# Performance work log

Measured on AMD Instinct MI355X. Metric: run time of the kernel, lower is better.

The kernel has to match this reference:

```python
import jax, jax.numpy as jnp
import numpy as np

N_TOKEN = 267735
D_EMBED = 1024
D_PROJ = 1024
DIV_VAL = 4
CUTOFFS = [20000, 40000, 200000, N_TOKEN]   # cutoffs + [n_token]
ENDS = [0] + CUTOFFS                         # cutoff_ends
N_CLUSTERS = len(CUTOFFS) - 1                # 3
HEAD_SIZE = CUTOFFS[0] + N_CLUSTERS          # 20003
N = 1024                                     # len*bsz


def setup_inputs() -> dict:
    key = jax.random.key(0)
    ks = jax.random.split(key, 16)
    d_embs = [D_EMBED // DIV_VAL ** i for i in range(4)]  # 1024,256,64,16
    sizes = [HEAD_SIZE] + [ENDS[i + 1] - ENDS[i] for i in range(1, 4)]  # 20003,20000,160000,67735
    s = 0.02
    inp = {
        'hidden': jax.random.normal(ks[0], (N, D_PROJ), dtype=jnp.float32),
        'target': jax.random.randint(ks[1], (N,), 0, N_TOKEN, dtype=jnp.int32),
    }
    for i in range(4):
        inp[f'w{i}'] = jax.random.normal(ks[2 + 3 * i], (sizes[i], d_embs[i]), dtype=jnp.float32) * s
        inp[f'b{i}'] = jnp.zeros((sizes[i],), dtype=jnp.float32)
        inp[f'p{i}'] = jax.random.normal(ks[3 + 3 * i], (D_PROJ, d_embs[i]), dtype=jnp.float32) * s
    return inp


def _logit(h, w, b, p):
    # F.linear(hidden, proj.t()) -> h @ p ; F.linear(., weight, bias) -> @ w.T + b
    return (h @ p) @ w.T + b


def reference(hidden, target, w0, b0, p0, w1, b1, p1, w2, b2, p2, w3, b3, p3):
    head_lp = jax.nn.log_softmax(_logit(hidden, w0, b0, p0), axis=1)  # [N, HEAD_SIZE]
    tails = [(w1, b1, p1), (w2, b2, p2), (w3, b3, p3)]
    lps = []
    # shortlist cluster: gather target logprob directly from head
    t0 = jnp.clip(target, 0, CUTOFFS[0] - 1)
    lps.append(jnp.take_along_axis(head_lp, t0[:, None], axis=1)[:, 0])
    # tail clusters: small projected matmul + log_softmax + gather, combined with cluster logprob head_lp[:, -i]
    for i in range(1, 4):
        l, r = ENDS[i], ENDS[i + 1]
        ti = jnp.clip(target - l, 0, r - l - 1)
        tail_lp = jax.nn.log_softmax(_logit(hidden, *tails[i - 1]), axis=1)  # [N, r-l]
        lps.append(head_lp[:, -i] + jnp.take_along_axis(tail_lp, ti[:, None], axis=1)[:, 0])
    masks = [(target >= ENDS[i]) & (target < ENDS[i + 1]) for i in range(4)]
    logprob = jnp.select(masks, lps)
    return -logprob  # [N] per-token NLL, original order (keep_order=True)
```

## Files before the change

### kernel.cpp

```cpp
#include <hip/hip_runtime.h>
#include <hip/hip_bf16.h>
#include <math.h>

#define NTOK 1024
#define DPROJ 1024
#define PSTRIDE 1376
#define HEADS 20003
#define LOG2E 1.4426950408889634f
#define LN2   0.6931471805599453f
#define WSCALE (4.0f * LOG2E)
#define PSCALE 0.25f

#if __has_builtin(__builtin_amdgcn_exp2f)
#define EXP2(x) __builtin_amdgcn_exp2f(x)
#else
#define EXP2(x) exp2f(x)
#endif

#define MFMA8(a, b, c) __builtin_amdgcn_mfma_f32_16x16x32_fp8_fp8(a, b, c, 0, 0, 0)

typedef __attribute__((ext_vector_type(8))) short bf16x8;
typedef __attribute__((ext_vector_type(4))) float f32x4;
typedef long long i64;
typedef __attribute__((ext_vector_type(2))) long long i64x2;

__device__ __forceinline__ short f2bf(float f) {
    unsigned u = __float_as_uint(f);
    u += 0x7fffu + ((u >> 16) & 1u);
    return (short)(u >> 16);
}
__device__ __forceinline__ unsigned pk4fp8(float a, float b, float c, float d) {
    unsigned v = __builtin_amdgcn_cvt_pk_fp8_f32(a, b, 0, false);
    v = __builtin_amdgcn_cvt_pk_fp8_f32(c, d, v, true);
    return v;
}
__device__ __forceinline__ unsigned char fp8_1(float a) {
    return (unsigned char)(__builtin_amdgcn_cvt_pk_fp8_f32(a, a, 0, false) & 0xff);
}
__device__ __forceinline__ i64 wfrag(const float* wp) {
    float4 x = *(const float4*)(wp);
    float4 y = *(const float4*)(wp + 4);
    unsigned lo = pk4fp8(x.x * WSCALE, x.y * WSCALE, x.z * WSCALE, x.w * WSCALE);
    unsigned hi = pk4fp8(y.x * WSCALE, y.y * WSCALE, y.z * WSCALE, y.w * WSCALE);
    return (i64)(((unsigned long long)hi << 32) | lo);
}

#define NB0H 313
#define NB1T 157
#define NB2T 313
#define NB3T 133
#define NSLAB (NB0H + NB1T + NB2T + NB3T)

#define EB0N 20096
#define EB1N 20096
#define EB2N 160256
#define EB3N 68096
#define EBTOT (EB0N + EB1N + EB2N + EB3N)

__global__ __launch_bounds__(256) void prep(const float* __restrict__ hidden,
                                            const float* __restrict__ p0,
                                            const float* __restrict__ p1,
                                            const float* __restrict__ p2,
                                            const float* __restrict__ p3,
                                            const float* __restrict__ b0,
                                            const float* __restrict__ b1,
                                            const float* __restrict__ b2,
                                            const float* __restrict__ b3,
                                            short* __restrict__ hbP,
                                            short* __restrict__ pTbP0,
                                            short* __restrict__ pTbP1,
                                            short* __restrict__ pTbP2,
                                            short* __restrict__ pTbP3,
                                            float* __restrict__ sums,
                                            unsigned char* __restrict__ pk3,
                                            float* __restrict__ eb0,
                                            float* __restrict__ eb1,
                                            float* __restrict__ eb2,
                                            float* __restrict__ eb3) {
    __shared__ float tile[64][65];
    int bid = blockIdx.x, tid = threadIdx.x;
    if (bid >= 418) {
        int g = (bid - 418) * 256 + tid;
        if (g < EB0N) {
            eb0[g] = (g < HEADS) ? exp2f(b0[g] * LOG2E) : 0.f;
        } else if (g < EB0N + EB1N) {
            int i = g - EB0N;
            eb1[i] = (i < 20000) ? exp2f(b1[i] * LOG2E) : 0.f;
        } else if (g < EB0N + EB1N + EB2N) {
            int i = g - EB0N - EB1N;
            eb2[i] = (i < 160000) ? exp2f(b2[i] * LOG2E) : 0.f;
        } else if (g < EBTOT) {
            int i = g - EB0N - EB1N - EB2N;
            eb3[i] = (i < 67735) ? exp2f(b3[i] * LOG2E) : 0.f;
        }
        return;
    }
    if (bid == 416) {
        float4 z = {0.f, 0.f, 0.f, 0.f};
        #pragma unroll
        for (int i = 0; i < 4; ++i) *((float4*)sums + i * 256 + tid) = z;
        return;
    }
    if (bid == 417) {
        int4 z = {0, 0, 0, 0};
        #pragma unroll
        for (int i = 0; i < 8; ++i) *((int4*)pk3 + i * 256 + tid) = z;
        return;
    }
    if (bid < 64) {
        int tt = bid;
        #pragma unroll
        for (int q = 0; q < 8; ++q) {
            int fi = q * 256 + tid;
            int l = fi & 63;
            int row = tt * 16 + (l & 15);
            int kb = (fi >> 6) * 32 + (l >> 4) * 8;
            const float* hp = hidden + row * 1024 + kb;
            float4 x = *(const float4*)hp;
            float4 y = *(const float4*)(hp + 4);
            bf16x8 o;
            o[0]=f2bf(x.x); o[1]=f2bf(x.y); o[2]=f2bf(x.z); o[3]=f2bf(x.w);
            o[4]=f2bf(y.x); o[5]=f2bf(y.y); o[6]=f2bf(y.z); o[7]=f2bf(y.w);
            *(bf16x8*)(hbP + (size_t)tt * 16384 + fi * 8) = o;
        }
        return;
    }
    int lb = bid - 64;
    const float* p; short* dst; int d, kt, jb;
    if (lb < 256)      { p = p0; dst = pTbP0; d = 1024; kt = lb >> 4; jb = lb & 15; }
    else if (lb < 320) { lb -= 256; p = p1; dst = pTbP1; d = 256; kt = lb >> 2; jb = lb & 3; }
    else if (lb < 336) { lb -= 320; p = p2; dst = pTbP2; d = 64;  kt = lb; jb = 0; }
    else               { lb -= 336; p = p3; dst = pTbP3; d = 16;  kt = lb; jb = 0; }
    int k0 = kt * 64, j0 = jb * 64;
    int tx = tid & 63, ty = tid >> 6;
    #pragma unroll
    for (int rr = 0; rr < 16; ++rr) {
        int k = k0 + ty * 16 + rr;
        int j = j0 + tx;
        if (j < d) tile[ty * 16 + rr][tx] = p[k * d + j];
    }
    __syncthreads();
    int ch = tid >> 5;
    int jtl = ch >> 1, ksl = ch & 1;
    int jt = jb * 4 + jtl;
    if (jt * 16 < d) {
        #pragma unroll
        for (int li = 0; li < 2; ++li) {
            int l = (tid & 31) + li * 32;
            int jl = jtl * 16 + (l & 15);
            int kl = ksl * 32 + (l >> 4) * 8;
            bf16x8 o;
            #pragma unroll
            for (int e = 0; e < 8; ++e) o[e] = f2bf(tile[kl + e][jl]);
            *(bf16x8*)(dst + ((size_t)jt * 32 + kt * 2 + ksl) * 512 + l * 8) = o;
        }
    }
}

__global__ __launch_bounds__(256) void proj(const short* __restrict__ hbP,
                                            const short* __restrict__ pTbP0,
                                            const short* __restrict__ pTbP1,
                                            const short* __restrict__ pTbP2,
                                            const short* __restrict__ pTbP3,
                                            float* __restrict__ projf,
                                            unsigned char* __restrict__ pk0,
                                            unsigned char* __restrict__ pk1,
                                            unsigned char* __restrict__ pk2,
                                            unsigned char* __restrict__ pk3) {
    __shared__ float spackf[16][72];
    __shared__ unsigned char sp8[1024];
    int tt = blockIdx.x, jbG = blockIdx.y, tid = threadIdx.x;
    const short* pB; unsigned char* pkc; int d, KSp, coloff, jb;
    if (jbG < 16)      { pB = pTbP0; pkc = pk0; d = 1024; KSp = 32; coloff = 0;    jb = jbG; }
    else if (jbG < 20) { pB = pTbP1; pkc = pk1; d = 256;  KSp = 8;  coloff = 1024; jb = jbG - 16; }
    else if (jbG == 20){ pB = pTbP2; pkc = pk2; d = 64;   KSp = 2;  coloff = 1280; jb = 0; }
    else               { pB = pTbP3; pkc = pk3; d = 16;   KSp = 1;  coloff = 1344; jb = 0; }
    int w = tid >> 6, lane = tid & 63;
    int l16 = lane & 15, quad = lane >> 4;
    int jt = jb * 4 + w;
    if (jt * 16 < d) {
        const short* ap = hbP + ((size_t)tt * 32) * 512 + lane * 8;
        const short* bp = pB  + ((size_t)jt * 32) * 512 + lane * 8;
        f32x4 x0 = {0,0,0,0}, x1 = {0,0,0,0};
        #pragma unroll
        for (int ks = 0; ks < 16; ++ks) {
            bf16x8 a0 = *(const bf16x8*)(ap + ks * 512);
            bf16x8 b0 = *(const bf16x8*)(bp + ks * 512);
            bf16x8 a1 = *(const bf16x8*)(ap + (ks + 16) * 512);
            bf16x8 b1 = *(const bf16x8*)(bp + (ks + 16) * 512);
            x0 = __builtin_amdgcn_mfma_f32_16x16x32_bf16(a0, b0, x0, 0, 0, 0);
            x1 = __builtin_amdgcn_mfma_f32_16x16x32_bf16(a1, b1, x1, 0, 0, 0);
        }
        f32x4 acc = x0 + x1;
        int kk = w * 16 + l16;
        #pragma unroll
        for (int r = 0; r < 4; ++r) {
            int tok = quad * 4 + r;
            spackf[tok][kk] = acc[r];
            int idx;
            if (d > 16) idx = ((kk & 31) >> 3) * 256 + tok * 16 + (kk >> 5) * 8 + (kk & 7);
            else        idx = ((kk & 31) >> 3) * 128 + tok * 8 + (kk & 7);
            sp8[idx] = fp8_1(acc[r] * PSCALE);
        }
    }
    __syncthreads();
    int j0g = jb * 64;
    int dcols = min(64, d - j0g);
    {
        int row = tid >> 4, cb = (tid & 15) * 4;
        if (cb < dcols) {
            float4 v = *(const float4*)&spackf[row][cb];
            *(float4*)&projf[(tt * 16 + row) * PSTRIDE + coloff + j0g + cb] = v;
        }
    }
    {
        int nbytes = 16 * dcols;
        if (tid * 4 < nbytes) {
            unsigned char* gdst = pkc + ((size_t)tt * KSp + (j0g >> 5)) * 512;
            *(unsigned*)(gdst + tid * 4) = *(const unsigned*)(sp8 + tid * 4);
        }
    }
}

__device__ __forceinline__ void stage16k(const unsigned char* g, unsigned char* l,
                                         int wave, int lane) {
    const unsigned char* gs = g + wave * 4096 + lane * 16;
    unsigned char* ls = l + wave * 4096;
    #pragma unroll
    for (int i = 0; i < 4; ++i)
        __builtin_amdgcn_global_load_lds(
            (const __attribute__((address_space(1))) unsigned*)(gs + i * 1024),
            (__attribute__((address_space(3))) unsigned*)(ls + i * 1024), 16, 0, 0);
}

__device__ __forceinline__ void lse_head(const float* __restrict__ w,
                                         const float* __restrict__ eb,
                                         const unsigned char* __restrict__ pk,
                                         float* __restrict__ part, int bid,
                                         unsigned char (*sbuf)[16384], float* bsum) {
    int tid = threadIdx.x;
    int wave = tid >> 6, lane = tid & 63;
    int quad = lane >> 4, l16 = lane & 15;
    int v0 = bid * 64 + wave * 16;

    for (int i = tid; i < NTOK; i += 256) bsum[i] = 0.f;

    i64 areg[32];
    float ee[4];
    int va = v0 + l16;
    #pragma unroll
    for (int ks = 0; ks < 32; ++ks)
        areg[ks] = (va < HEADS) ? wfrag(w + (long)va * 1024 + ks * 32 + quad * 8) : 0;
    #pragma unroll
    for (int r = 0; r < 4; ++r)
        ee[r] = eb[v0 + quad * 4 + r];

    unsigned char* pA = sbuf[0];
    unsigned char* pB = sbuf[1];
    unsigned char* pS = sbuf[2];
    stage16k(pk, pA, wave, lane);
    stage16k(pk + 16384, pB, wave, lane);
    __syncthreads();
    for (int tt = 0; tt < 64; ++tt) {
        if (tt + 2 < 64) stage16k(pk + (size_t)(tt + 2) * 16384, pS, wave, lane);
        const unsigned char* sb = pA;
        f32x4 x0 = {0,0,0,0}, x1 = x0;
        __builtin_amdgcn_s_setprio(1);
        #pragma unroll
        for (int p = 0; p < 16; ++p) {
            i64x2 b2 = *(const i64x2*)(sb + p * 1024 + lane * 16);
            x0 = MFMA8(areg[2 * p],     b2[0], x0);
            x1 = MFMA8(areg[2 * p + 1], b2[1], x1);
        }
        __builtin_amdgcn_s_setprio(0);
        f32x4 a = x0 + x1;
        float e0 = EXP2(a[0]) * ee[0] + EXP2(a[2]) * ee[2];
        float e1 = EXP2(a[1]) * ee[1] + EXP2(a[3]) * ee[3];
        float e = e0 + e1;
        e += __shfl_xor(e, 16, 64);
        e += __shfl_xor(e, 32, 64);
        if (lane < 16) atomicAdd(&bsum[tt * 16 + lane], e);
        __syncthreads();
        unsigned char* t = pA; pA = pB; pB = pS; pS = t;
    }
    *((float4*)part + tid) = *((const float4*)bsum + tid);
}

template <int KS, int VT>
__device__ __forceinline__ void lse_tail(const float* __restrict__ w,
                                         const float* __restrict__ eb,
                                         const unsigned char* __restrict__ pk,
                                         float* __restrict__ part,
                                         int V, int D, int bid, float* bsum) {
    int tid = threadIdx.x;
    int wave = tid >> 6, lane = tid & 63;
    int quad = lane >> 4, l16 = lane & 15;
    int v0 = bid * (64 * VT) + wave * (16 * VT);

    for (int i = tid; i < NTOK; i += 256) bsum[i] = 0.f;
    __syncthreads();

    i64 areg[VT][KS];
    float ee[VT][4];
    #pragma unroll
    for (int vt = 0; vt < VT; ++vt) {
        int va = v0 + vt * 16 + l16;
        #pragma unroll
        for (int ks = 0; ks < KS; ++ks) {
            int k = ks * 32 + quad * 8;
            areg[vt][ks] = (va < V && k < D) ? wfrag(w + (long)va * D + k) : 0;
        }
        #pragma unroll
        for (int r = 0; r < 4; ++r)
            ee[vt][r] = eb[v0 + vt * 16 + quad * 4 + r];
    }

    if constexpr (KS >= 2) {
        constexpr int KSP = KS / 2;
        i64x2 bn[KSP], bc[KSP];
        #pragma unroll
        for (int p = 0; p < KSP; ++p)
            bn[p] = *(const i64x2*)(pk + p * 1024 + lane * 16);
        for (int tt = 0; tt < 64; ++tt) {
            #pragma unroll
            for (int p = 0; p < KSP; ++p) bc[p] = bn[p];
            if (tt < 63) {
                const unsigned char* nb = pk + (size_t)(tt + 1) * (KS * 512);
                #pragma unroll
                for (int p = 0; p < KSP; ++p)
                    bn[p] = *(const i64x2*)(nb + p * 1024 + lane * 16);
            }
            f32x4 accs[VT];
            __builtin_amdgcn_s_setprio(1);
            #pragma unroll
            for (int vt = 0; vt < VT; ++vt) {
                if constexpr (KS >= 4) {
                    f32x4 y0 = {0,0,0,0}, y1 = {0,0,0,0};
                    #pragma unroll
                    for (int p = 0; p < KSP; ++p) {
                        y0 = MFMA8(areg[vt][2 * p],     bc[p][0], y0);
                        y1 = MFMA8(areg[vt][2 * p + 1], bc[p][1], y1);
                    }
                    accs[vt] = y0 + y1;
                } else {
                    f32x4 y = {0,0,0,0};
                    y = MFMA8(areg[vt][0], bc[0][0], y);
                    y = MFMA8(areg[vt][1], bc[0][1], y);
                    accs[vt] = y;
                }
            }
            __builtin_amdgcn_s_setprio(0);
            float e0 = 0.f, e1 = 0.f;
            #pragma unroll
            for (int vt = 0; vt < VT; ++vt) {
                e0 += EXP2(accs[vt][0]) * ee[vt][0];
                e1 += EXP2(accs[vt][1]) * ee[vt][1];
                e0 += EXP2(accs[vt][2]) * ee[vt][2];
                e1 += EXP2(accs[vt][3]) * ee[vt][3];
            }
            float e = e0 + e1;
            e += __shfl_xor(e, 16, 64);
            e += __shfl_xor(e, 32, 64);
            if (lane < 16) atomicAdd(&bsum[tt * 16 + lane], e);
        }
    } else {
        i64 bn = *(const i64*)(pk + lane * 8);
        for (int tt = 0; tt < 64; ++tt) {
            i64 bc = bn;
            if (tt < 63) bn = *(const i64*)(pk + (size_t)(tt + 1) * 512 + lane * 8);
            f32x4 accs[VT];
            __builtin_amdgcn_s_setprio(1);
            #pragma unroll
            for (int vt = 0; vt < VT; ++vt) {
                f32x4 y0 = {0,0,0,0};
                accs[vt] = MFMA8(areg[vt][0], bc, y0);
            }
            __builtin_amdgcn_s_setprio(0);
            float e0 = 0.f, e1 = 0.f;
            #pragma unroll
            for (int vt = 0; vt < VT; ++vt) {
                e0 += EXP2(accs[vt][0]) * ee[vt][0];
                e1 += EXP2(accs[vt][1]) * ee[vt][1];
                e0 += EXP2(accs[vt][2]) * ee[vt][2];
                e1 += EXP2(accs[vt][3]) * ee[vt][3];
            }
            float e = e0 + e1;
            e += __shfl_xor(e, 16, 64);
            e += __shfl_xor(e, 32, 64);
            if (lane < 16) atomicAdd(&bsum[tt * 16 + lane], e);
        }
    }
    __syncthreads();
    *((float4*)part + tid) = *((const float4*)bsum + tid);
}

__global__ __launch_bounds__(256, 2) void lse_all(const float* __restrict__ w0, const float* __restrict__ eb0,
                                                  const float* __restrict__ w1, const float* __restrict__ eb1,
                                                  const float* __restrict__ w2, const float* __restrict__ eb2,
                                                  const float* __restrict__ w3, const float* __restrict__ eb3,
                                                  const unsigned char* __restrict__ pk0,
                                                  const unsigned char* __restrict__ pk1,
                                                  const unsigned char* __restrict__ pk2,
                                                  const unsigned char* __restrict__ pk3,
                                                  float* __restrict__ part) {
    __shared__ unsigned char sbuf[3][16384];
    __shared__ float bsum[NTOK];
    int bid = blockIdx.x;
    float* slab = part + (size_t)bid * NTOK;
    if (bid < NB0H) {
        lse_head(w0, eb0, pk0, slab, bid, sbuf, bsum);
    } else if (bid < NB0H + NB1T) {
        lse_tail<8, 2>(w1, eb1, pk1, slab, 20000,  256, bid - NB0H, bsum);
    } else if (bid < NB0H + NB1T + NB2T) {
        lse_tail<2, 8>(w2, eb2, pk2, slab, 160000, 64,  bid - NB0H - NB1T, bsum);
    } else {
        lse_tail<1, 8>(w3, eb3, pk3, slab, 67735,  16,  bid - NB0H - NB1T - NB2T, bsum);
    }
}

__global__ __launch_bounds__(256) void reduce_part(const float* __restrict__ part,
                                                   float* __restrict__ sums) {
    int bid = blockIdx.x;
    int c = bid >> 5, rem = bid & 31, q = rem >> 3, sl = rem & 7;
    const int off[4] = {0, NB0H, NB0H + NB1T, NB0H + NB1T + NB2T};
    const int cnt[4] = {NB0H, NB1T, NB2T, NB3T};
    int tok = q * 256 + threadIdx.x;
    const float* p = part + (size_t)off[c] * NTOK + tok;
    int n = cnt[c];
    float s0 = 0.f, s1 = 0.f, s2 = 0.f, s3 = 0.f;
    int b = sl;
    for (; b + 24 < n; b += 32) {
        s0 += p[(size_t)b * NTOK];
        s1 += p[(size_t)(b + 8) * NTOK];
        s2 += p[(size_t)(b + 16) * NTOK];
        s3 += p[(size_t)(b + 24) * NTOK];
    }
    for (; b < n; b += 8) s0 += p[(size_t)b * NTOK];
    float s = (s0 + s1) + (s2 + s3);
    atomicAdd(&sums[c * NTOK + tok], s);
}

__global__ __launch_bounds__(256) void finalize(const int* __restrict__ target,
                                                const float* __restrict__ projf,
                                                const float* __restrict__ sums,
                                                const float* __restrict__ w0, const float* __restrict__ b0,
                                                const float* __restrict__ w1, const float* __restrict__ b1,
                                                const float* __restrict__ w2, const float* __restrict__ b2,
                                                const float* __restrict__ w3, const float* __restrict__ b3,
                                                float* __restrict__ out) {
    int wave = threadIdx.x >> 6, lane = threadIdx.x & 63;
    int row = blockIdx.x * 4 + wave;
    int t = target[row];
    int c = (t < 20000) ? 0 : (t < 40000) ? 1 : (t < 200000) ? 2 : 3;
    int col0 = (c == 0) ? t : (HEADS - c);
    const float* pr = projf + row * PSTRIDE;

    float s = 0.f;
    for (int k = lane; k < DPROJ; k += 64) s += pr[k] * w0[col0 * DPROJ + k];
    #pragma unroll
    for (int off = 32; off; off >>= 1) s += __shfl_xor(s, off, 64);
    float hl = s + b0[col0];
    float lse0 = __log2f(sums[row]) * LN2;

    float res;
    if (c == 0) {
        res = lse0 - hl;
    } else {
        const float* wc; const float* bc; int d, coloff, l;
        if (c == 1)      { wc = w1; bc = b1; d = 256; coloff = 1024; l = 20000; }
        else if (c == 2) { wc = w2; bc = b2; d = 64;  coloff = 1280; l = 40000; }
        else             { wc = w3; bc = b3; d = 16;  coloff = 1344; l = 200000; }
        int tc = t - l;
        float s2 = 0.f;
        for (int k = lane; k < d; k += 64) s2 += pr[coloff + k] * wc[tc * d + k];
        #pragma unroll
        for (int off = 32; off; off >>= 1) s2 += __shfl_xor(s2, off, 64);
        float tl = s2 + bc[tc];
        float lsec = __log2f(sums[c * NTOK + row]) * LN2;
        res = lse0 - hl + lsec - tl;
    }
    if (lane == 0) out[row] = res;
}


extern "C" void kernel_launch(void* const* d_in, const int* in_sizes, int n_in,
                              void* d_out, int out_size, void* d_ws, size_t ws_size,
                              hipStream_t stream) {
    const float* hidden = (const float*)d_in[0];
    const int*   target = (const int*)d_in[1];
    const float* w0 = (const float*)d_in[2];
    const float* b0 = (const float*)d_in[3];
    const float* p0 = (const float*)d_in[4];
    const float* w1 = (const float*)d_in[5];
    const float* b1 = (const float*)d_in[6];
    const float* p1 = (const float*)d_in[7];
    const float* w2 = (const float*)d_in[8];
    const float* b2 = (const float*)d_in[9];
    const float* p2 = (const float*)d_in[10];
    const float* w3 = (const float*)d_in[11];
    const float* b3 = (const float*)d_in[12];
    const float* p3 = (const float*)d_in[13];

    short* base = (short*)d_ws;
    short* hbP   = base;
    short* pTbP0 = base + 1048576;
    short* pTbP1 = base + 2097152;
    short* pTbP2 = base + 2359296;
    short* pTbP3 = base + 2424832;
    float* projf = (float*)((char*)d_ws + 4882432);
    unsigned char* pk0 = (unsigned char*)d_ws + 10518528;
    unsigned char* pk1 = pk0 + 1048576;
    unsigned char* pk2 = pk1 + 262144;
    unsigned char* pk3 = pk2 + 65536;
    float* sums  = (float*)((char*)d_ws + 11927552);
    float* part  = (float*)((char*)d_ws + 11943936);
    float* eb0   = (float*)((char*)d_ws + 15695872);
    float* eb1   = (float*)((char*)d_ws + 15776256);
    float* eb2   = (float*)((char*)d_ws + 15856640);
    float* eb3   = (float*)((char*)d_ws + 16497664);

    prep<<<1467, 256, 0, stream>>>(hidden, p0, p1, p2, p3, b0, b1, b2, b3,
                                   hbP, pTbP0, pTbP1, pTbP2, pTbP3, sums, pk3,
                                   eb0, eb1, eb2, eb3);
    proj<<<dim3(64, 22), 256, 0, stream>>>(hbP, pTbP0, pTbP1, pTbP2, pTbP3,
                                           projf, pk0, pk1, pk2, pk3);
    lse_all<<<NSLAB, 256, 0, stream>>>(w0, eb0, w1, eb1, w2, eb2, w3, eb3,
                                       pk0, pk1, pk2, pk3, part);
    reduce_part<<<128, 256, 0, stream>>>(part, sums);
    finalize<<<256, 256, 0, stream>>>(target, projf, sums,
                                      w0, b0, w1, b1, w2, b2, w3, b3, (float*)d_out);
}
```

Before: 305.1 us.

## Fuse bias exponentiation into LSE kernels and fold partial reduction into finalize

Drops the bias-exp precompute blocks from prep and computes exp(bias) inline inside the head and tail LSE kernels. Removes the separate reduce_part kernel and the zeroing of sums; finalize now sums the per-slab partials for each row directly with a wave reduction. This cuts one kernel launch and some global round-trips. In exchange each finalize wave reads several hundred strided partial values, which is an uncoalesced access pattern.

```diff
diff --git a/kernel.cpp b/kernel.cpp
--- a/kernel.cpp
+++ b/kernel.cpp
@@ -51,56 +51,20 @@
 #define NB3T 133
 #define NSLAB (NB0H + NB1T + NB2T + NB3T)
 
-#define EB0N 20096
-#define EB1N 20096
-#define EB2N 160256
-#define EB3N 68096
-#define EBTOT (EB0N + EB1N + EB2N + EB3N)
-
 __global__ __launch_bounds__(256) void prep(const float* __restrict__ hidden,
                                             const float* __restrict__ p0,
                                             const float* __restrict__ p1,
                                             const float* __restrict__ p2,
                                             const float* __restrict__ p3,
-                                            const float* __restrict__ b0,
-                                            const float* __restrict__ b1,
-                                            const float* __restrict__ b2,
-                                            const float* __restrict__ b3,
                                             short* __restrict__ hbP,
                                             short* __restrict__ pTbP0,
                                             short* __restrict__ pTbP1,
                                             short* __restrict__ pTbP2,
                                             short* __restrict__ pTbP3,
-                                            float* __restrict__ sums,
-                                            unsigned char* __restrict__ pk3,
-                                            float* __restrict__ eb0,
-                                            float* __restrict__ eb1,
-                                            float* __restrict__ eb2,
-                                            float* __restrict__ eb3) {
+                                            unsigned char* __restrict__ pk3) {
     __shared__ float tile[64][65];
     int bid = blockIdx.x, tid = threadIdx.x;
-    if (bid >= 418) {
-        int g = (bid - 418) * 256 + tid;
-        if (g < EB0N) {
-            eb0[g] = (g < HEADS) ? exp2f(b0[g] * LOG2E) : 0.f;
-        } else if (g < EB0N + EB1N) {
-            int i = g - EB0N;
-            eb1[i] = (i < 20000) ? exp2f(b1[i] * LOG2E) : 0.f;
-        } else if (g < EB0N + EB1N + EB2N) {
-            int i = g - EB0N - EB1N;
-            eb2[i] = (i < 160000) ? exp2f(b2[i] * LOG2E) : 0.f;
-        } else if (g < EBTOT) {
-            int i = g - EB0N - EB1N - EB2N;
-            eb3[i] = (i < 67735) ? exp2f(b3[i] * LOG2E) : 0.f;
-        }
-        return;
-    }
-    if (bid == 416) {
-        float4 z = {0.f, 0.f, 0.f, 0.f};
-        #pragma unroll
-        for (int i = 0; i < 4; ++i) *((float4*)sums + i * 256 + tid) = z;
-        return;
-    }
+    if (bid == 416) return;
     if (bid == 417) {
         int4 z = {0, 0, 0, 0};
         #pragma unroll
@@ -234,7 +198,7 @@
 }
 
 __device__ __forceinline__ void lse_head(const float* __restrict__ w,
-                                         const float* __restrict__ eb,
+                                         const float* __restrict__ bias,
                                          const unsigned char* __restrict__ pk,
                                          float* __restrict__ part, int bid,
                                          unsigned char (*sbuf)[16384], float* bsum) {
@@ -252,8 +216,10 @@
     for (int ks = 0; ks < 32; ++ks)
         areg[ks] = (va < HEADS) ? wfrag(w + (long)va * 1024 + ks * 32 + quad * 8) : 0;
     #pragma unroll
-    for (int r = 0; r < 4; ++r)
-        ee[r] = eb[v0 + quad * 4 + r];
+    for (int r = 0; r < 4; ++r) {
+        int vb = v0 + quad * 4 + r;
+        ee[r] = (vb < HEADS) ? EXP2(bias[vb] * LOG2E) : 0.f;
+    }
 
     unsigned char* pA = sbuf[0];
     unsigned char* pB = sbuf[1];
@@ -288,7 +254,7 @@
 
 template <int KS, int VT>
 __device__ __forceinline__ void lse_tail(const float* __restrict__ w,
-                                         const float* __restrict__ eb,
+                                         const float* __restrict__ bias,
                                          const unsigned char* __restrict__ pk,
                                          float* __restrict__ part,
                                          int V, int D, int bid, float* bsum) {
@@ -311,8 +277,10 @@
             areg[vt][ks] = (va < V && k < D) ? wfrag(w + (long)va * D + k) : 0;
         }
         #pragma unroll
-        for (int r = 0; r < 4; ++r)
-            ee[vt][r] = eb[v0 + vt * 16 + quad * 4 + r];
+        for (int r = 0; r < 4; ++r) {
+            int vb = v0 + vt * 16 + quad * 4 + r;
+            ee[vt][r] = (vb < V) ? EXP2(bias[vb] * LOG2E) : 0.f;
+        }
     }
 
     if constexpr (KS >= 2) {
@@ -394,10 +362,10 @@
     *((float4*)part + tid) = *((const float4*)bsum + tid);
 }
 
-__global__ __launch_bounds__(256, 2) void lse_all(const float* __restrict__ w0, const float* __restrict__ eb0,
-                                                  const float* __restrict__ w1, const float* __restrict__ eb1,
-                                                  const float* __restrict__ w2, const float* __restrict__ eb2,
-                                                  const float* __restrict__ w3, const float* __restrict__ eb3,
+__global__ __launch_bounds__(256, 2) void lse_all(const float* __restrict__ w0, const float* __restrict__ b0,
+                                                  const float* __restrict__ w1, const float* __restrict__ b1,
+                                                  const float* __restrict__ w2, const float* __restrict__ b2,
+                                                  const float* __restrict__ w3, const float* __restrict__ b3,
                                                   const unsigned char* __restrict__ pk0,
                                                   const unsigned char* __restrict__ pk1,
                                                   const unsigned char* __restrict__ pk2,
@@ -408,41 +376,19 @@
     int bid = blockIdx.x;
     float* slab = part + (size_t)bid * NTOK;
     if (bid < NB0H) {
-        lse_head(w0, eb0, pk0, slab, bid, sbuf, bsum);
+        lse_head(w0, b0, pk0, slab, bid, sbuf, bsum);
     } else if (bid < NB0H + NB1T) {
-        lse_tail<8, 2>(w1, eb1, pk1, slab, 20000,  256, bid - NB0H, bsum);
+        lse_tail<8, 2>(w1, b1, pk1, slab, 20000,  256, bid - NB0H, bsum);
     } else if (bid < NB0H + NB1T + NB2T) {
-        lse_tail<2, 8>(w2, eb2, pk2, slab, 160000, 64,  bid - NB0H - NB1T, bsum);
+        lse_tail<2, 8>(w2, b2, pk2, slab, 160000, 64,  bid - NB0H - NB1T, bsum);
     } else {
-        lse_tail<1, 8>(w3, eb3, pk3, slab, 67735,  16,  bid - NB0H - NB1T - NB2T, bsum);
-    }
-}
-
-__global__ __launch_bounds__(256) void reduce_part(const float* __restrict__ part,
-                                                   float* __restrict__ sums) {
-    int bid = blockIdx.x;
-    int c = bid >> 5, rem = bid & 31, q = rem >> 3, sl = rem & 7;
-    const int off[4] = {0, NB0H, NB0H + NB1T, NB0H + NB1T + NB2T};
-    const int cnt[4] = {NB0H, NB1T, NB2T, NB3T};
-    int tok = q * 256 + threadIdx.x;
-    const float* p = part + (size_t)off[c] * NTOK + tok;
-    int n = cnt[c];
-    float s0 = 0.f, s1 = 0.f, s2 = 0.f, s3 = 0.f;
-    int b = sl;
-    for (; b + 24 < n; b += 32) {
-        s0 += p[(size_t)b * NTOK];
-        s1 += p[(size_t)(b + 8) * NTOK];
-        s2 += p[(size_t)(b + 16) * NTOK];
-        s3 += p[(size_t)(b + 24) * NTOK];
-    }
-    for (; b < n; b += 8) s0 += p[(size_t)b * NTOK];
-    float s = (s0 + s1) + (s2 + s3);
-    atomicAdd(&sums[c * NTOK + tok], s);
+        lse_tail<1, 8>(w3, b3, pk3, slab, 67735,  16,  bid - NB0H - NB1T - NB2T, bsum);
+    }
 }
 
 __global__ __launch_bounds__(256) void finalize(const int* __restrict__ target,
                                                 const float* __restrict__ projf,
-                                                const float* __restrict__ sums,
+                                                const float* __restrict__ part,
                                                 const float* __restrict__ w0, const float* __restrict__ b0,
                                                 const float* __restrict__ w1, const float* __restrict__ b1,
                                                 const float* __restrict__ w2, const float* __restrict__ b2,
@@ -455,31 +401,47 @@
     int col0 = (c == 0) ? t : (HEADS - c);
     const float* pr = projf + row * PSTRIDE;
 
-    float s = 0.f;
-    for (int k = lane; k < DPROJ; k += 64) s += pr[k] * w0[col0 * DPROJ + k];
-    #pragma unroll
-    for (int off = 32; off; off >>= 1) s += __shfl_xor(s, off, 64);
-    float hl = s + b0[col0];
-    float lse0 = __log2f(sums[row]) * LN2;
-
-    float res;
-    if (c == 0) {
-        res = lse0 - hl;
-    } else {
-        const float* wc; const float* bc; int d, coloff, l;
-        if (c == 1)      { wc = w1; bc = b1; d = 256; coloff = 1024; l = 20000; }
-        else if (c == 2) { wc = w2; bc = b2; d = 64;  coloff = 1280; l = 40000; }
-        else             { wc = w3; bc = b3; d = 16;  coloff = 1344; l = 200000; }
-        int tc = t - l;
-        float s2 = 0.f;
+    float hs = 0.f, cs = 0.f;
+    for (int s = lane; s < NB0H; s += 64) hs += part[(size_t)s * NTOK + row];
+    if (c > 0) {
+        int off = (c == 1) ? NB0H : (c == 2) ? NB0H + NB1T : NB0H + NB1T + NB2T;
+        int cnt = (c == 1) ? NB1T : (c == 2) ? NB2T : NB3T;
+        for (int s = lane; s < cnt; s += 64) cs += part[(size_t)(off + s) * NTOK + row];
+    }
+
+    float s0 = 0.f;
+    for (int k = lane; k < DPROJ; k += 64) s0 += pr[k] * w0[col0 * DPROJ + k];
+
+    float s2 = 0.f;
+    const float* wc = w1; const float* bc = b1; int d = 256, coloff = 1024, l = 20000;
+    if (c == 2)      { wc = w2; bc = b2; d = 64;  coloff = 1280; l = 40000; }
+    else if (c == 3) { wc = w3; bc = b3; d = 16;  coloff = 1344; l = 200000; }
+    int tc = t - l;
+    if (c > 0) {
         for (int k = lane; k < d; k += 64) s2 += pr[coloff + k] * wc[tc * d + k];
-        #pragma unroll
-        for (int off = 32; off; off >>= 1) s2 += __shfl_xor(s2, off, 64);
-        float tl = s2 + bc[tc];
-        float lsec = __log2f(sums[c * NTOK + row]) * LN2;
-        res = lse0 - hl + lsec - tl;
-    }
-    if (lane == 0) out[row] = res;
+    }
+
+    #pragma unroll
+    for (int off = 32; off; off >>= 1) {
+        hs += __shfl_xor(hs, off, 64);
+        cs += __shfl_xor(cs, off, 64);
+        s0 += __shfl_xor(s0, off, 64);
+        s2 += __shfl_xor(s2, off, 64);
+    }
+
+    if (lane == 0) {
+        float hl = s0 + b0[col0];
+        float lse0 = __log2f(hs) * LN2;
+        float res;
+        if (c == 0) {
+            res = lse0 - hl;
+        } else {
+            float tl = s2 + bc[tc];
+            float lsec = __log2f(cs) * LN2;
+            res = lse0 - hl + lsec - tl;
+        }
+        out[row] = res;
+    }
 }
 
 
@@ -512,21 +474,14 @@
     unsigned char* pk1 = pk0 + 1048576;
     unsigned char* pk2 = pk1 + 262144;
     unsigned char* pk3 = pk2 + 65536;
-    float* sums  = (float*)((char*)d_ws + 11927552);
     float* part  = (float*)((char*)d_ws + 11943936);
-    float* eb0   = (float*)((char*)d_ws + 15695872);
-    float* eb1   = (float*)((char*)d_ws + 15776256);
-    float* eb2   = (float*)((char*)d_ws + 15856640);
-    float* eb3   = (float*)((char*)d_ws + 16497664);
-
-    prep<<<1467, 256, 0, stream>>>(hidden, p0, p1, p2, p3, b0, b1, b2, b3,
-                                   hbP, pTbP0, pTbP1, pTbP2, pTbP3, sums, pk3,
-                                   eb0, eb1, eb2, eb3);
+
+    prep<<<418, 256, 0, stream>>>(hidden, p0, p1, p2, p3,
+                                  hbP, pTbP0, pTbP1, pTbP2, pTbP3, pk3);
     proj<<<dim3(64, 22), 256, 0, stream>>>(hbP, pTbP0, pTbP1, pTbP2, pTbP3,
                                            projf, pk0, pk1, pk2, pk3);
-    lse_all<<<NSLAB, 256, 0, stream>>>(w0, eb0, w1, eb1, w2, eb2, w3, eb3,
+    lse_all<<<NSLAB, 256, 0, stream>>>(w0, b0, w1, b1, w2, b2, w3, b3,
                                        pk0, pk1, pk2, pk3, part);
-    reduce_part<<<128, 256, 0, stream>>>(part, sums);
-    finalize<<<256, 256, 0, stream>>>(target, projf, sums,
+    finalize<<<256, 256, 0, stream>>>(target, projf, part,
                                       w0, b0, w1, b1, w2, b2, w3, b3, (float*)d_out);
 }
```

Measured after the change: 309.5 us. Within noise of the previous version (+1.5%).
